# Kernel tuning notes

Measured on AMD Instinct MI355X. Metric: run time of the kernel, lower is better.

## Reference

```python
import jax, jax.numpy as jnp
import numpy as np

H, E, K = 1024, 8, 2  # hidden_size, num_experts, top_k
B, S = 2, 4096


def setup_inputs() -> dict:
    key = jax.random.key(0)
    ks = jax.random.split(key, 5)
    s = 1.0 / np.sqrt(H)
    return {
        "x": jax.random.normal(ks[0], (B, S, H), dtype=jnp.float32),
        "ln_scale": jnp.ones((H,), jnp.float32),
        "ln_bias": jnp.zeros((H,), jnp.float32),
        "w1": (jax.random.normal(ks[1], (H, H), jnp.float32) * s),
        "b1": jnp.zeros((H,), jnp.float32),
        "w2": (jax.random.normal(ks[2], (H, E), jnp.float32) * s),
        "b2": jnp.zeros((E,), jnp.float32),
        "We": (jax.random.normal(ks[3], (E, H, H), jnp.float32) * s),
        "be": jnp.zeros((E, H), jnp.float32),
    }


def _layernorm(x, scale, bias, eps=1e-5):
    m = jnp.mean(x, axis=-1, keepdims=True)
    v = jnp.var(x, axis=-1, keepdims=True)
    return (x - m) * jax.lax.rsqrt(v + eps) * scale + bias


def reference(x, ln_scale, ln_bias, w1, b1, w2, b2, We, be):
    b, s, h = x.shape
    # --- router (BaseRouter): LN -> MLP -> softmax -> top-k -> renorm ---
    xn = _layernorm(x, ln_scale, ln_bias)
    hmid = jax.nn.relu(xn @ w1 + b1)
    logits = hmid @ w2 + b2                      # [B,S,E]
    probs = jax.nn.softmax(logits, axis=-1)
    topk_p, topk_i = jax.lax.top_k(probs, K)     # [B,S,K]
    topk_p = topk_p / jnp.sum(topk_p, axis=-1, keepdims=True)
    # sparse combine weights [B,S,E]: renormalized top-k gate, 0 elsewhere
    cw = jnp.sum(topk_p[..., None] * jax.nn.one_hot(topk_i, E, dtype=x.dtype), axis=-2)
    # --- expert dispatch / weighted combine ---
    t = b * s
    xf = x.reshape(t, h)
    cwf = cw.reshape(t, E)
    ye = jnp.einsum('th,ehd->etd', xf, We) + be[:, None, :]   # [E,T,H]
    out = jnp.einsum('te,etd->td', cwf, ye).reshape(b, s, h)
    # --- aux load-balance loss ---
    mean_p = jnp.mean(probs, axis=(0, 1))        # [E]
    aux = jnp.sum(mean_p * jnp.log(mean_p * E + 1e-9))
    return out, aux
```

## Files before the change

kernel.cpp:

```cpp
#include <hip/hip_runtime.h>
#include <hip/hip_fp16.h>

#define H 1024
#define E 8
#define TT 8192

typedef __attribute__((ext_vector_type(8))) short bf16x8;
typedef __attribute__((ext_vector_type(4))) float f32x4;

__device__ __forceinline__ unsigned short f2bf(float f) {
  unsigned int u = __float_as_uint(f);
  u += 0x7fffu + ((u >> 16) & 1u);
  return (unsigned short)(u >> 16);
}

__device__ __forceinline__ int swz(int row, int c) {
  return (row << 5) | (((c ^ (row >> 1)) & 3) << 3);
}

__device__ __forceinline__ void gld16(void* lds, const void* g) {
  __builtin_amdgcn_global_load_lds((const __attribute__((address_space(1))) void*)g,
                                   (__attribute__((address_space(3))) void*)lds, 16, 0, 0);
}

__global__ __launch_bounds__(64) void k_init(int* cnt, double* psum) {
  int t = threadIdx.x;
  if (t < E) { cnt[t] = 0; psum[t] = 0.0; }
}

__global__ __launch_bounds__(256) void k_cast_we(const float* __restrict__ we, unsigned short* __restrict__ wet) {
  __shared__ unsigned short tile[32][33];
  int e = blockIdx.z;
  int kb = blockIdx.x << 5, nb = blockIdx.y << 5;
  int t = threadIdx.x;
  int cc = t & 31, rr = t >> 5;
  size_t base = (size_t)e * H * H;
#pragma unroll
  for (int r = 0; r < 4; ++r) {
    int k = kb + rr + (r << 3);
    tile[rr + (r << 3)][cc] = f2bf(we[base + (size_t)k * H + nb + cc]);
  }
  __syncthreads();
#pragma unroll
  for (int r = 0; r < 4; ++r) {
    int n = nb + rr + (r << 3);
    wet[base + (size_t)n * H + kb + cc] = tile[cc][rr + (r << 3)];
  }
}

__global__ __launch_bounds__(256) void k_cast_w1(const float* __restrict__ w1, const float* __restrict__ lsc,
                                                 unsigned short* __restrict__ w1h, unsigned short* __restrict__ w1l) {
  __shared__ float tile[32][33];
  int kb = blockIdx.x << 5, nb = blockIdx.y << 5;
  int t = threadIdx.x;
  int cc = t & 31, rr = t >> 5;
#pragma unroll
  for (int r = 0; r < 4; ++r) {
    int k = kb + rr + (r << 3);
    tile[rr + (r << 3)][cc] = w1[(size_t)k * H + nb + cc] * lsc[k];
  }
  __syncthreads();
#pragma unroll
  for (int r = 0; r < 4; ++r) {
    int n = nb + rr + (r << 3);
    float v = tile[cc][rr + (r << 3)];
    unsigned short h = f2bf(v);
    float hv = __uint_as_float((unsigned)h << 16);
    unsigned short l = f2bf(v - hv);
    w1h[(size_t)n * H + kb + cc] = h;
    w1l[(size_t)n * H + kb + cc] = l;
  }
}

__global__ __launch_bounds__(256) void k_b1a(const float* __restrict__ w1, const float* __restrict__ lbi,
                                             float* __restrict__ part) {
  int bk = blockIdx.x, t = threadIdx.x;
  float a0 = 0, a1 = 0, a2 = 0, a3 = 0;
  for (int kk = 0; kk < 16; ++kk) {
    int k = (bk << 4) + kk;
    float lb = lbi[k];
    const float* row = &w1[(size_t)k * H];
    a0 = fmaf(lb, row[t], a0);
    a1 = fmaf(lb, row[t + 256], a1);
    a2 = fmaf(lb, row[t + 512], a2);
    a3 = fmaf(lb, row[t + 768], a3);
  }
  part[bk * H + t] = a0;
  part[bk * H + t + 256] = a1;
  part[bk * H + t + 512] = a2;
  part[bk * H + t + 768] = a3;
}

__global__ __launch_bounds__(256) void k_b1b(const float* __restrict__ part, const float* __restrict__ b1,
                                             float* __restrict__ b1eff) {
  int n = (blockIdx.x << 8) + threadIdx.x;
  float s = b1[n];
  for (int j = 0; j < 64; ++j) s += part[j * H + n];
  b1eff[n] = s;
}

__global__ __launch_bounds__(256) void k_stats(const float* __restrict__ x, float2* __restrict__ stats,
                                               unsigned short* __restrict__ xb) {
  int tok = blockIdx.x, t = threadIdx.x;
  const float4 v = *reinterpret_cast<const float4*>(&x[(size_t)tok * H + (t << 2)]);
  float s = v.x + v.y + v.z + v.w;
  float ss = v.x * v.x + v.y * v.y + v.z * v.z + v.w * v.w;
#pragma unroll
  for (int off = 32; off; off >>= 1) { s += __shfl_down(s, off); ss += __shfl_down(ss, off); }
  __shared__ float red[4][2];
  int lane = t & 63, wv = t >> 6;
  if (lane == 0) { red[wv][0] = s; red[wv][1] = ss; }
  __syncthreads();
  float fs = red[0][0] + red[1][0] + red[2][0] + red[3][0];
  float fss = red[0][1] + red[1][1] + red[2][1] + red[3][1];
  float mean = fs * (1.0f / H);
  float var = fss * (1.0f / H) - mean * mean;
  float rstd = rsqrtf(var + 1e-5f);
  if (t == 0) stats[tok] = make_float2(mean, rstd);
  ushort4 ob;
  ob.x = f2bf(v.x); ob.y = f2bf(v.y); ob.z = f2bf(v.z); ob.w = f2bf(v.w);
  *reinterpret_cast<ushort4*>(&xb[(size_t)tok * H + (t << 2)]) = ob;
}

__global__ __launch_bounds__(256) void k_router_mfma(
    const float* __restrict__ x, const float2* __restrict__ stats,
    const unsigned short* __restrict__ w1h, const unsigned short* __restrict__ w1l,
    const float* __restrict__ b1eff, const float* __restrict__ w2, float* __restrict__ plog) {
  __shared__ __align__(16) short At[2][8192];
  __shared__ __align__(16) short Bt[2][8192];
  int t = threadIdx.x;
  int bm = blockIdx.x << 7, bn = blockIdx.y << 7;
  int w = t >> 6, lane = t & 63;
  int s0 = (w << 8) + lane;
  int r0_ = s0 >> 2, cg0 = (s0 & 3) ^ ((r0_ >> 1) & 3);
  int s1 = s0 + 64, r1_ = s1 >> 2, cg1 = (s1 & 3) ^ ((r1_ >> 1) & 3);
  int s2 = s0 + 128, r2_ = s2 >> 2, cg2 = (s2 & 3) ^ ((r2_ >> 1) & 3);
  int s3 = s0 + 192, r3_ = s3 >> 2, cg3 = (s3 & 3) ^ ((r3_ >> 1) & 3);
  const unsigned short* srcB0 =
      ((r0_ < 128) ? &w1h[(size_t)(bn + r0_) * H] : &w1l[(size_t)(bn + r0_ - 128) * H]) + (cg0 << 3);
  const unsigned short* srcB1 =
      ((r1_ < 128) ? &w1h[(size_t)(bn + r1_) * H] : &w1l[(size_t)(bn + r1_ - 128) * H]) + (cg1 << 3);
  const unsigned short* srcB2 =
      ((r2_ < 128) ? &w1h[(size_t)(bn + r2_) * H] : &w1l[(size_t)(bn + r2_ - 128) * H]) + (cg2 << 3);
  const unsigned short* srcB3 =
      ((r3_ < 128) ? &w1h[(size_t)(bn + r3_) * H] : &w1l[(size_t)(bn + r3_ - 128) * H]) + (cg3 << 3);
  int dB0 = (w << 11), dB1 = dB0 + 512, dB2 = dB0 + 1024, dB3 = dB0 + 1536;
  int arow = t >> 1, ac0 = (t & 1) << 1;
  float2 mr = stats[bm + arow];
  float rsc = mr.y, mb = -mr.x * mr.y;
  const float* xsrc = &x[(size_t)(bm + arow) * H + (ac0 << 3)];
  int wA0 = swz(arow, ac0), wA1 = swz(arow, ac0 + 1);
  int wL0 = swz(arow + 128, ac0), wL1 = swz(arow + 128, ac0 + 1);
  float4 va0, va1, va2, va3;
  auto ldx = [&]() {
    va0 = *(const float4*)(xsrc + 0); va1 = *(const float4*)(xsrc + 4);
    va2 = *(const float4*)(xsrc + 8); va3 = *(const float4*)(xsrc + 12);
  };
  auto split_store = [&](int b) {
    float zz[16];
    zz[0] = fmaf(va0.x, rsc, mb); zz[1] = fmaf(va0.y, rsc, mb);
    zz[2] = fmaf(va0.z, rsc, mb); zz[3] = fmaf(va0.w, rsc, mb);
    zz[4] = fmaf(va1.x, rsc, mb); zz[5] = fmaf(va1.y, rsc, mb);
    zz[6] = fmaf(va1.z, rsc, mb); zz[7] = fmaf(va1.w, rsc, mb);
    zz[8] = fmaf(va2.x, rsc, mb); zz[9] = fmaf(va2.y, rsc, mb);
    zz[10] = fmaf(va2.z, rsc, mb); zz[11] = fmaf(va2.w, rsc, mb);
    zz[12] = fmaf(va3.x, rsc, mb); zz[13] = fmaf(va3.y, rsc, mb);
    zz[14] = fmaf(va3.z, rsc, mb); zz[15] = fmaf(va3.w, rsc, mb);
    unsigned hw[8], lw[8];
#pragma unroll
    for (int p = 0; p < 8; ++p) {
      unsigned ua = __float_as_uint(zz[2 * p]), ub = __float_as_uint(zz[2 * p + 1]);
      hw[p] = (ua >> 16) | (ub & 0xffff0000u);
      float la = zz[2 * p] - __uint_as_float(ua & 0xffff0000u);
      float lb = zz[2 * p + 1] - __uint_as_float(ub & 0xffff0000u);
      lw[p] = (__float_as_uint(la) >> 16) | (__float_as_uint(lb) & 0xffff0000u);
    }
    *(int4*)&At[b][wA0] = make_int4(hw[0], hw[1], hw[2], hw[3]);
    *(int4*)&At[b][wA1] = make_int4(hw[4], hw[5], hw[6], hw[7]);
    *(int4*)&At[b][wL0] = make_int4(lw[0], lw[1], lw[2], lw[3]);
    *(int4*)&At[b][wL1] = make_int4(lw[4], lw[5], lw[6], lw[7]);
  };
  int wr = (w >> 1) << 6, wc = (w & 1) << 6;
  int l15 = lane & 15, lgp = lane >> 4;
  f32x4 acc[4][4];
#pragma unroll
  for (int i = 0; i < 4; ++i)
#pragma unroll
    for (int j = 0; j < 4; ++j) acc[i][j] = f32x4{0.f, 0.f, 0.f, 0.f};
  ldx();
  gld16(&Bt[0][dB0], srcB0); gld16(&Bt[0][dB1], srcB1);
  gld16(&Bt[0][dB2], srcB2); gld16(&Bt[0][dB3], srcB3);
  split_store(0);
  asm volatile("s_waitcnt vmcnt(0) lgkmcnt(0)" ::: "memory");
  __builtin_amdgcn_s_barrier();
  for (int kt = 0; kt < 32; ++kt) {
    int b = kt & 1;
    if (kt < 31) {
      xsrc += 32;
      ldx();
      srcB0 += 32; srcB1 += 32; srcB2 += 32; srcB3 += 32;
      gld16(&Bt[b ^ 1][dB0], srcB0); gld16(&Bt[b ^ 1][dB1], srcB1);
      gld16(&Bt[b ^ 1][dB2], srcB2); gld16(&Bt[b ^ 1][dB3], srcB3);
    }
    bf16x8 bh[4], bl[4];
#pragma unroll
    for (int j = 0; j < 4; ++j) {
      bh[j] = *(const bf16x8*)&Bt[b][swz(wc + (j << 4) + l15, lgp)];
      bl[j] = *(const bf16x8*)&Bt[b][swz(128 + wc + (j << 4) + l15, lgp)];
    }
#pragma unroll
    for (int i = 0; i < 4; ++i) {
      bf16x8 ah = *(const bf16x8*)&At[b][swz(wr + (i << 4) + l15, lgp)];
      bf16x8 al = *(const bf16x8*)&At[b][swz(128 + wr + (i << 4) + l15, lgp)];
#pragma unroll
      for (int j = 0; j < 4; ++j) {
        acc[i][j] = __builtin_amdgcn_mfma_f32_16x16x32_bf16(ah, bh[j], acc[i][j], 0, 0, 0);
        acc[i][j] = __builtin_amdgcn_mfma_f32_16x16x32_bf16(ah, bl[j], acc[i][j], 0, 0, 0);
        acc[i][j] = __builtin_amdgcn_mfma_f32_16x16x32_bf16(al, bh[j], acc[i][j], 0, 0, 0);
      }
    }
    if (kt < 31) split_store(b ^ 1);
    asm volatile("s_waitcnt vmcnt(0) lgkmcnt(0)" ::: "memory");
    __builtin_amdgcn_s_barrier();
  }
  float w2r[4][8], b1r[4];
#pragma unroll
  for (int j = 0; j < 4; ++j) {
    int col = bn + wc + (j << 4) + l15;
    float4 p0 = *(const float4*)&w2[(size_t)col * E];
    float4 p1 = *(const float4*)&w2[(size_t)col * E + 4];
    w2r[j][0] = p0.x; w2r[j][1] = p0.y; w2r[j][2] = p0.z; w2r[j][3] = p0.w;
    w2r[j][4] = p1.x; w2r[j][5] = p1.y; w2r[j][6] = p1.z; w2r[j][7] = p1.w;
    b1r[j] = b1eff[col];
  }
#pragma unroll
  for (int i = 0; i < 4; ++i)
#pragma unroll
    for (int j = 0; j < 4; ++j)
#pragma unroll
      for (int r = 0; r < 4; ++r) acc[i][j][r] = fmaxf(acc[i][j][r] + b1r[j], 0.f);
  int wh = wc >> 6;
  size_t pbase = ((size_t)(blockIdx.y * 2 + wh) * TT + bm) * E;
#pragma unroll
  for (int e = 0; e < E; ++e) {
    float se[4][4];
#pragma unroll
    for (int i = 0; i < 4; ++i)
#pragma unroll
      for (int r = 0; r < 4; ++r)
        se[i][r] = acc[i][0][r] * w2r[0][e] + acc[i][1][r] * w2r[1][e] +
                   acc[i][2][r] * w2r[2][e] + acc[i][3][r] * w2r[3][e];
#pragma unroll
    for (int off = 1; off < 16; off <<= 1)
#pragma unroll
      for (int i = 0; i < 4; ++i)
#pragma unroll
        for (int r = 0; r < 4; ++r) se[i][r] += __shfl_xor(se[i][r], off);
    if (l15 == 0) {
#pragma unroll
      for (int i = 0; i < 4; ++i)
#pragma unroll
        for (int r = 0; r < 4; ++r) {
          int row = wr + (i << 4) + (lgp << 2) + r;
          plog[pbase + (size_t)row * E + e] = se[i][r];
        }
    }
  }
}

__global__ __launch_bounds__(256) void k_top(const float* __restrict__ plog, const float* __restrict__ b2,
                                             int* __restrict__ topE, float* __restrict__ topW,
                                             int* __restrict__ listIdx, float* __restrict__ listW,
                                             int* __restrict__ cnt, double* __restrict__ psum) {
  int t = threadIdx.x, lane = t & 63;
  int tok = (blockIdx.x << 8) + t;
  float lg[E], p[E];
  float4 ba = *reinterpret_cast<const float4*>(b2);
  float4 bb = *reinterpret_cast<const float4*>(b2 + 4);
  lg[0] = ba.x; lg[1] = ba.y; lg[2] = ba.z; lg[3] = ba.w;
  lg[4] = bb.x; lg[5] = bb.y; lg[6] = bb.z; lg[7] = bb.w;
#pragma unroll
  for (int nb = 0; nb < 16; ++nb) {
    const float* pp = &plog[((size_t)nb * TT + tok) * E];
    float4 q0 = *reinterpret_cast<const float4*>(pp);
    float4 q1 = *reinterpret_cast<const float4*>(pp + 4);
    lg[0] += q0.x; lg[1] += q0.y; lg[2] += q0.z; lg[3] += q0.w;
    lg[4] += q1.x; lg[5] += q1.y; lg[6] += q1.z; lg[7] += q1.w;
  }
  float m = lg[0];
#pragma unroll
  for (int e = 1; e < E; ++e) m = fmaxf(m, lg[e]);
  float s = 0.f;
#pragma unroll
  for (int e = 0; e < E; ++e) { p[e] = __expf(lg[e] - m); s += p[e]; }
  float inv = 1.f / s;
#pragma unroll
  for (int e = 0; e < E; ++e) p[e] *= inv;
  {
    float ps[E];
#pragma unroll
    for (int e = 0; e < E; ++e) ps[e] = p[e];
#pragma unroll
    for (int off = 1; off < 64; off <<= 1)
#pragma unroll
      for (int e = 0; e < E; ++e) ps[e] += __shfl_xor(ps[e], off);
    if (lane == 0)
#pragma unroll
      for (int e = 0; e < E; ++e) atomicAdd(&psum[e], (double)ps[e]);
  }
  int e0 = 0;
#pragma unroll
  for (int e = 1; e < E; ++e) if (p[e] > p[e0]) e0 = e;
  int e1 = (e0 == 0) ? 1 : 0;
#pragma unroll
  for (int e = 0; e < E; ++e) if (e != e0 && p[e] > p[e1]) e1 = e;
  float rsw = 1.f / (p[e0] + p[e1]);
  float w0 = p[e0] * rsw, w1v = p[e1] * rsw;
  topE[tok << 1] = e0; topE[(tok << 1) + 1] = e1;
  topW[tok << 1] = w0; topW[(tok << 1) + 1] = w1v;
  unsigned long long lt = (1ull << lane) - 1ull;
#pragma unroll
  for (int e = 0; e < E; ++e) {
    unsigned long long m0 = __ballot(e0 == e);
    unsigned long long m1 = __ballot(e1 == e);
    int n0 = __popcll(m0), total = n0 + __popcll(m1);
    if (total == 0) continue;
    int leader = __ffsll(m0 | m1) - 1;
    int base = 0;
    if (lane == leader) base = atomicAdd(&cnt[e], total);
    base = __shfl(base, leader);
    if (e0 == e) {
      int pos = e * TT + base + __popcll(m0 & lt);
      listIdx[pos] = (tok << 1); listW[pos] = w0;
    }
    if (e1 == e) {
      int pos = e * TT + base + n0 + __popcll(m1 & lt);
      listIdx[pos] = (tok << 1) | 1; listW[pos] = w1v;
    }
  }
}

__global__ __launch_bounds__(256) void k_expert_gemm(const unsigned short* __restrict__ xb,
                                                     const unsigned short* __restrict__ wet,
                                                     const int* __restrict__ listIdx, const float* __restrict__ listW,
                                                     const int* __restrict__ cnt, unsigned short* __restrict__ ys) {
  int e = blockIdx.z;
  int c = cnt[e];
  int r0 = blockIdx.x << 7;
  if (r0 >= c) return;
  int n0 = blockIdx.y << 7;
  __shared__ __align__(16) short A[2][4096], B[2][4096];
  __shared__ int gi[128];
  __shared__ float gw[128];
  int t = threadIdx.x;
  if (t < 128) {
    int rr = r0 + t;
    gi[t] = (rr < c) ? listIdx[e * TT + rr] : -1;
    gw[t] = (rr < c) ? listW[e * TT + rr] : 0.f;
  }
  __syncthreads();
  int w = t >> 6, lane = t & 63;
  int s0 = (w << 7) + lane, s1 = s0 + 64;
  int rA0 = s0 >> 2, cg0 = (s0 & 3) ^ ((rA0 >> 1) & 3);
  int rA1 = s1 >> 2, cg1 = (s1 & 3) ^ ((rA1 >> 1) & 3);
  int pk0 = gi[rA0], pk1 = gi[rA1];
  const unsigned short* srcA0 = &xb[(size_t)((pk0 < 0) ? 0 : (pk0 >> 1)) * H + (cg0 << 3)];
  const unsigned short* srcA1 = &xb[(size_t)((pk1 < 0) ? 0 : (pk1 >> 1)) * H + (cg1 << 3)];
  size_t wbase = (size_t)e * H * H;
  const unsigned short* srcB0 = &wet[wbase + (size_t)(n0 + rA0) * H + (cg0 << 3)];
  const unsigned short* srcB1 = &wet[wbase + (size_t)(n0 + rA1) * H + (cg1 << 3)];
  int d0 = (w << 10), d1 = d0 + 512;
  int wr = (w >> 1) << 6, wc = (w & 1) << 6;
  int l15 = lane & 15, lgp = lane >> 4;
  f32x4 acc[4][4];
#pragma unroll
  for (int i = 0; i < 4; ++i)
#pragma unroll
    for (int j = 0; j < 4; ++j) acc[i][j] = f32x4{0.f, 0.f, 0.f, 0.f};
  gld16(&A[0][d0], srcA0); gld16(&A[0][d1], srcA1);
  gld16(&B[0][d0], srcB0); gld16(&B[0][d1], srcB1);
  asm volatile("s_waitcnt vmcnt(0)" ::: "memory");
  __builtin_amdgcn_s_barrier();
  for (int kt = 0; kt < 32; ++kt) {
    int b = kt & 1;
    if (kt < 31) {
      srcA0 += 32; srcA1 += 32; srcB0 += 32; srcB1 += 32;
      gld16(&A[b ^ 1][d0], srcA0); gld16(&A[b ^ 1][d1], srcA1);
      gld16(&B[b ^ 1][d0], srcB0); gld16(&B[b ^ 1][d1], srcB1);
    }
    bf16x8 bq[4];
#pragma unroll
    for (int j = 0; j < 4; ++j) bq[j] = *(const bf16x8*)&B[b][swz(wc + (j << 4) + l15, lgp)];
#pragma unroll
    for (int i = 0; i < 4; ++i) {
      bf16x8 af = *(const bf16x8*)&A[b][swz(wr + (i << 4) + l15, lgp)];
#pragma unroll
      for (int j = 0; j < 4; ++j)
        acc[i][j] = __builtin_amdgcn_mfma_f32_16x16x32_bf16(af, bq[j], acc[i][j], 0, 0, 0);
    }
    asm volatile("s_waitcnt vmcnt(0) lgkmcnt(0)" ::: "memory");
    __builtin_amdgcn_s_barrier();
  }
#pragma unroll
  for (int i = 0; i < 4; ++i) {
#pragma unroll
    for (int r = 0; r < 4; ++r) {
      int row = wr + (i << 4) + (lgp << 2) + r;
      int pk = gi[row];
      if (pk < 0) continue;
      int tok = pk >> 1, slot = pk & 1;
      float wgt = gw[row];
      size_t ob = ((size_t)slot * TT + tok) * H + n0 + wc + l15;
#pragma unroll
      for (int j = 0; j < 4; ++j) ys[ob + (j << 4)] = __half_as_ushort(__float2half(wgt * acc[i][j][r]));
    }
  }
}

__global__ __launch_bounds__(256) void k_combine(const unsigned short* __restrict__ ys, const int* __restrict__ topE,
                                                 const float* __restrict__ topW, const float* __restrict__ be,
                                                 float* __restrict__ out) {
  int tok = blockIdx.x, t = threadIdx.x;
  int e0 = topE[tok << 1], e1 = topE[(tok << 1) + 1];
  float w0 = topW[tok << 1], w1v = topW[(tok << 1) + 1];
  int h = t << 2;
  size_t base = (size_t)tok * H + h;
  ushort4 a = *reinterpret_cast<const ushort4*>(&ys[base]);
  ushort4 b = *reinterpret_cast<const ushort4*>(&ys[(size_t)TT * H + base]);
  float4 b0 = *reinterpret_cast<const float4*>(&be[e0 * H + h]);
  float4 b1v = *reinterpret_cast<const float4*>(&be[e1 * H + h]);
  float4 o;
  o.x = __half2float(__ushort_as_half(a.x)) + __half2float(__ushort_as_half(b.x)) + w0 * b0.x + w1v * b1v.x;
  o.y = __half2float(__ushort_as_half(a.y)) + __half2float(__ushort_as_half(b.y)) + w0 * b0.y + w1v * b1v.y;
  o.z = __half2float(__ushort_as_half(a.z)) + __half2float(__ushort_as_half(b.z)) + w0 * b0.z + w1v * b1v.z;
  o.w = __half2float(__ushort_as_half(a.w)) + __half2float(__ushort_as_half(b.w)) + w0 * b0.w + w1v * b1v.w;
  *reinterpret_cast<float4*>(&out[base]) = o;
}

__global__ __launch_bounds__(64) void k_aux(const double* __restrict__ psum, float* __restrict__ outAux) {
  if (threadIdx.x == 0) {
    double a = 0.0;
    for (int e = 0; e < E; ++e) {
      double mp = psum[e] / (double)TT;
      a += mp * log(mp * (double)E + 1e-9);
    }
    outAux[0] = (float)a;
  }
}

extern "C" void kernel_launch(void* const* d_in, const int* in_sizes, int n_in, void* d_out, int out_size, void* d_ws,
                              size_t ws_size, hipStream_t stream) {
  const float* x = (const float*)d_in[0];
  const float* lsc = (const float*)d_in[1];
  const float* lbi = (const float*)d_in[2];
  const float* w1 = (const float*)d_in[3];
  const float* b1 = (const float*)d_in[4];
  const float* w2 = (const float*)d_in[5];
  const float* b2 = (const float*)d_in[6];
  const float* we = (const float*)d_in[7];
  const float* be = (const float*)d_in[8];
  float* out = (float*)d_out;
  char* ws = (char*)d_ws;

  char* p = ws;
  float2* stats = (float2*)p; p += TT * 8;
  int* topE = (int*)p; p += TT * 2 * 4;
  float* topW = (float*)p; p += TT * 2 * 4;
  int* listIdx = (int*)p; p += E * TT * 4;
  float* listW = (float*)p; p += E * TT * 4;
  int* cnt = (int*)p; p += 256;
  double* psum = (double*)p; p += 2048;
  float* b1eff = (float*)p; p += H * 4;
  float* part = (float*)p; p += 64 * H * 4;
  unsigned short* xb = (unsigned short*)(ws + (2u << 20));
  unsigned short* wet = (unsigned short*)(ws + (18u << 20));
  unsigned short* w1h = (unsigned short*)(ws + (34u << 20));
  unsigned short* w1l = (unsigned short*)(ws + (36u << 20));
  float* plog = (float*)(ws + (38u << 20));
  unsigned short* ys = (unsigned short*)(ws + (34u << 20));

  k_init<<<1, 64, 0, stream>>>(cnt, psum);
  k_cast_w1<<<dim3(32, 32), 256, 0, stream>>>(w1, lsc, w1h, w1l);
  k_b1a<<<64, 256, 0, stream>>>(w1, lbi, part);
  k_b1b<<<4, 256, 0, stream>>>(part, b1, b1eff);
  k_cast_we<<<dim3(32, 32, E), 256, 0, stream>>>(we, wet);
  k_stats<<<TT, 256, 0, stream>>>(x, stats, xb);
  k_router_mfma<<<dim3(TT / 128, H / 128), 256, 0, stream>>>(x, stats, w1h, w1l, b1eff, w2, plog);
  k_top<<<TT / 256, 256, 0, stream>>>(plog, b2, topE, topW, listIdx, listW, cnt, psum);
  k_expert_gemm<<<dim3(TT / 128, H / 128, E), 256, 0, stream>>>(xb, wet, listIdx, listW, cnt, ys);
  k_combine<<<TT, 256, 0, stream>>>(ys, topE, topW, be, out);
  k_aux<<<1, 64, 0, stream>>>(psum, out + (size_t)TT * H);
}
```

Baseline: 241.0 us.

## Deepen GEMM pipelines with partial vmcnt waits and remap block order

```diff
diff --git a/kernel.cpp b/kernel.cpp
--- a/kernel.cpp
+++ b/kernel.cpp
@@ -129,7 +129,9 @@
   __shared__ __align__(16) short At[2][8192];
   __shared__ __align__(16) short Bt[2][8192];
   int t = threadIdx.x;
-  int bm = blockIdx.x << 7, bn = blockIdx.y << 7;
+  int d = blockIdx.x + (blockIdx.y << 6);
+  int l = ((d & 7) << 6) + (d >> 3);
+  int bm = (l & 63) << 7, bnb = l >> 6, bn = bnb << 7;
   int w = t >> 6, lane = t & 63;
   int s0 = (w << 8) + lane;
   int r0_ = s0 >> 2, cg0 = (s0 & 3) ^ ((r0_ >> 1) & 3);
@@ -152,9 +154,13 @@
   int wA0 = swz(arow, ac0), wA1 = swz(arow, ac0 + 1);
   int wL0 = swz(arow + 128, ac0), wL1 = swz(arow + 128, ac0 + 1);
   float4 va0, va1, va2, va3;
-  auto ldx = [&]() {
-    va0 = *(const float4*)(xsrc + 0); va1 = *(const float4*)(xsrc + 4);
-    va2 = *(const float4*)(xsrc + 8); va3 = *(const float4*)(xsrc + 12);
+  auto ldx = [&](int ko) {
+    va0 = *(const float4*)(xsrc + ko + 0); va1 = *(const float4*)(xsrc + ko + 4);
+    va2 = *(const float4*)(xsrc + ko + 8); va3 = *(const float4*)(xsrc + ko + 12);
+  };
+  auto stageB = [&](int b, int ko) {
+    gld16(&Bt[b][dB0], srcB0 + ko); gld16(&Bt[b][dB1], srcB1 + ko);
+    gld16(&Bt[b][dB2], srcB2 + ko); gld16(&Bt[b][dB3], srcB3 + ko);
   };
   auto split_store = [&](int b) {
     float zz[16];
@@ -187,21 +193,21 @@
   for (int i = 0; i < 4; ++i)
 #pragma unroll
     for (int j = 0; j < 4; ++j) acc[i][j] = f32x4{0.f, 0.f, 0.f, 0.f};
-  ldx();
-  gld16(&Bt[0][dB0], srcB0); gld16(&Bt[0][dB1], srcB1);
-  gld16(&Bt[0][dB2], srcB2); gld16(&Bt[0][dB3], srcB3);
+  ldx(0);
+  stageB(0, 0);
   split_store(0);
-  asm volatile("s_waitcnt vmcnt(0) lgkmcnt(0)" ::: "memory");
-  __builtin_amdgcn_s_barrier();
   for (int kt = 0; kt < 32; ++kt) {
     int b = kt & 1;
     if (kt < 31) {
-      xsrc += 32;
-      ldx();
-      srcB0 += 32; srcB1 += 32; srcB2 += 32; srcB3 += 32;
-      gld16(&Bt[b ^ 1][dB0], srcB0); gld16(&Bt[b ^ 1][dB1], srcB1);
-      gld16(&Bt[b ^ 1][dB2], srcB2); gld16(&Bt[b ^ 1][dB3], srcB3);
-    }
+      ldx((kt + 1) << 5);
+      stageB(b ^ 1, (kt + 1) << 5);
+    }
+    if (kt < 31) {
+      asm volatile("s_waitcnt vmcnt(8) lgkmcnt(0)" ::: "memory");
+    } else {
+      asm volatile("s_waitcnt vmcnt(0) lgkmcnt(0)" ::: "memory");
+    }
+    __builtin_amdgcn_s_barrier();
     bf16x8 bh[4], bl[4];
 #pragma unroll
     for (int j = 0; j < 4; ++j) {
@@ -219,9 +225,11 @@
         acc[i][j] = __builtin_amdgcn_mfma_f32_16x16x32_bf16(al, bh[j], acc[i][j], 0, 0, 0);
       }
     }
-    if (kt < 31) split_store(b ^ 1);
-    asm volatile("s_waitcnt vmcnt(0) lgkmcnt(0)" ::: "memory");
-    __builtin_amdgcn_s_barrier();
+    if (kt < 31) {
+      split_store(b ^ 1);
+      asm volatile("s_waitcnt lgkmcnt(0)" ::: "memory");
+      __builtin_amdgcn_s_barrier();
+    }
   }
   float w2r[4][8], b1r[4];
 #pragma unroll
@@ -240,7 +248,7 @@
 #pragma unroll
       for (int r = 0; r < 4; ++r) acc[i][j][r] = fmaxf(acc[i][j][r] + b1r[j], 0.f);
   int wh = wc >> 6;
-  size_t pbase = ((size_t)(blockIdx.y * 2 + wh) * TT + bm) * E;
+  size_t pbase = ((size_t)(bnb * 2 + wh) * TT + bm) * E;
 #pragma unroll
   for (int e = 0; e < E; ++e) {
     float se[4][4];
@@ -344,12 +352,14 @@
                                                      const unsigned short* __restrict__ wet,
                                                      const int* __restrict__ listIdx, const float* __restrict__ listW,
                                                      const int* __restrict__ cnt, unsigned short* __restrict__ ys) {
-  int e = blockIdx.z;
+  int d = blockIdx.x + (blockIdx.y << 6) + (blockIdx.z << 9);
+  int l = ((d & 7) << 9) + (d >> 3);
+  int e = l >> 9, by = (l >> 6) & 7, bx = l & 63;
   int c = cnt[e];
-  int r0 = blockIdx.x << 7;
+  int r0 = bx << 7;
   if (r0 >= c) return;
-  int n0 = blockIdx.y << 7;
-  __shared__ __align__(16) short A[2][4096], B[2][4096];
+  int n0 = by << 7;
+  __shared__ __align__(16) short A[3][4096], B[3][4096];
   __shared__ int gi[128];
   __shared__ float gw[128];
   int t = threadIdx.x;
@@ -377,17 +387,22 @@
   for (int i = 0; i < 4; ++i)
 #pragma unroll
     for (int j = 0; j < 4; ++j) acc[i][j] = f32x4{0.f, 0.f, 0.f, 0.f};
-  gld16(&A[0][d0], srcA0); gld16(&A[0][d1], srcA1);
-  gld16(&B[0][d0], srcB0); gld16(&B[0][d1], srcB1);
-  asm volatile("s_waitcnt vmcnt(0)" ::: "memory");
-  __builtin_amdgcn_s_barrier();
+#pragma unroll
+  for (int pt = 0; pt < 3; ++pt) {
+    int ko = pt << 5;
+    gld16(&A[pt][d0], srcA0 + ko); gld16(&A[pt][d1], srcA1 + ko);
+    gld16(&B[pt][d0], srcB0 + ko); gld16(&B[pt][d1], srcB1 + ko);
+  }
+  int b = 0;
   for (int kt = 0; kt < 32; ++kt) {
-    int b = kt & 1;
-    if (kt < 31) {
-      srcA0 += 32; srcA1 += 32; srcB0 += 32; srcB1 += 32;
-      gld16(&A[b ^ 1][d0], srcA0); gld16(&A[b ^ 1][d1], srcA1);
-      gld16(&B[b ^ 1][d0], srcB0); gld16(&B[b ^ 1][d1], srcB1);
-    }
+    if (kt <= 29) {
+      asm volatile("s_waitcnt vmcnt(8)" ::: "memory");
+    } else if (kt == 30) {
+      asm volatile("s_waitcnt vmcnt(4)" ::: "memory");
+    } else {
+      asm volatile("s_waitcnt vmcnt(0)" ::: "memory");
+    }
+    __builtin_amdgcn_s_barrier();
     bf16x8 bq[4];
 #pragma unroll
     for (int j = 0; j < 4; ++j) bq[j] = *(const bf16x8*)&B[b][swz(wc + (j << 4) + l15, lgp)];
@@ -398,8 +413,13 @@
       for (int j = 0; j < 4; ++j)
         acc[i][j] = __builtin_amdgcn_mfma_f32_16x16x32_bf16(af, bq[j], acc[i][j], 0, 0, 0);
     }
-    asm volatile("s_waitcnt vmcnt(0) lgkmcnt(0)" ::: "memory");
-    __builtin_amdgcn_s_barrier();
+    if (kt < 29) {
+      __builtin_amdgcn_s_barrier();
+      int ko = (kt + 3) << 5;
+      gld16(&A[b][d0], srcA0 + ko); gld16(&A[b][d1], srcA1 + ko);
+      gld16(&B[b][d0], srcB0 + ko); gld16(&B[b][d1], srcB1 + ko);
+    }
+    b = (b == 2) ? 0 : b + 1;
   }
 #pragma unroll
   for (int i = 0; i < 4; ++i) {
```

New measurement: 250.5 us. 1.04x slower.
